# Optimization experiments

Hardware: AMD Instinct MI355X
Metric: run time of the kernel (lower is better)

Reference implementation:

```python
import math
import jax, jax.numpy as jnp
import numpy as np

B, C, N, K = 16, 64, 2048, 20

def setup_inputs() -> dict:
    key = jax.random.key(0)
    x = jax.random.normal(key, (B, C, N), dtype=jnp.float32)
    local_idx = jnp.zeros((B, N), dtype=bool)  # unused in dgcnn variant
    return {"x": x, "k": K, "local_idx": local_idx}

def _gather_points(points, idx):
    # points: (B, N, C), idx: (B, N, k) -> (B, N, k, C)
    return jax.vmap(lambda p, i: p[i])(points, idx)

def reference(x, k, local_idx):
    b, c, n = x.shape
    xt = jnp.swapaxes(x, 1, 2)  # (B, N, C)
    # negative squared pairwise distance: -||xi||^2 + 2 xi.xj - ||xj||^2
    inner = 2.0 * jnp.einsum('bnc,bmc->bnm', xt, xt)
    xx = jnp.sum(xt * xt, axis=-1)  # (B, N)
    pd = -xx[:, :, None] + inner - xx[:, None, :]
    _, idx = jax.lax.top_k(pd, k)  # (B, N, k) nearest neighbors
    knn_x = _gather_points(xt, idx)  # (B, N, k, C)
    # per-channel topk over the k neighbors, then mean
    k2 = math.ceil(k * 2 / 3)
    vals = jax.lax.top_k(jnp.swapaxes(knn_x, 2, 3), k2)[0]  # (B, N, C, k2)
    x1 = jnp.mean(vals, axis=-1)  # (B, N, C)
    # gather smoothed features at neighbor indices
    feat = _gather_points(x1, idx)  # (B, N, k, C)
    x_exp = jnp.broadcast_to(xt[:, :, None, :], (b, n, k, c))
    feature = jnp.concatenate([feat - x_exp, x_exp], axis=-1)  # (B, N, k, 2C)
    feature = jnp.transpose(feature, (0, 3, 1, 2))  # (B, 2C, N, k)
    idx_flat = (idx + jnp.arange(b, dtype=idx.dtype)[:, None, None] * n).reshape(-1)
    return feature, idx_flat
```

## Files before the change

kernel.cpp:

```cpp
#include <hip/hip_runtime.h>
#include <cstdint>
#include <cstddef>
#include <math.h>

#define BB 16
#define CC 64
#define NN 2048
#define KK 20
#define K2 14
#define TQ 8
#define NC 26

__global__ __launch_bounds__(256) void prep_kernel(const float* __restrict__ x,
                                                   float* __restrict__ xt,
                                                   float* __restrict__ xxf,
                                                   double* __restrict__ xxd) {
    __shared__ float s_t[64][65];
    int b = blockIdx.x >> 5;
    int n0 = (blockIdx.x & 31) * 64;
    const float* xb = x + (size_t)b * CC * NN;
    int tid = threadIdx.x;
    int cq = tid >> 6;
    int nl = tid & 63;

#pragma unroll
    for (int r = 0; r < 16; ++r) {
        int c = r * 4 + cq;
        s_t[c][nl] = xb[c * NN + n0 + nl];
    }
    __syncthreads();

#pragma unroll
    for (int r = 0; r < 16; ++r) {
        int n = r * 4 + cq;
        xt[((size_t)b * NN + n0 + n) * CC + nl] = s_t[nl][n];
    }

    if (tid < 64) {
        double s = 0.0;
#pragma unroll
        for (int c = 0; c < CC; ++c) {
            double v = (double)s_t[c][tid];
            s += v * v;
        }
        xxd[b * NN + n0 + tid] = s;
        xxf[b * NN + n0 + tid] = (float)s;
    }
}

__global__ __launch_bounds__(512) void knn_kernel(const float* __restrict__ x,
                                                  const float* __restrict__ xt,
                                                  const float* __restrict__ xxf,
                                                  const double* __restrict__ xxd,
                                                  int* __restrict__ idx_ws,
                                                  float* __restrict__ idx_out) {
    __shared__ float s_pd[TQ][NN];
    __shared__ __align__(16) float s_q[CC][TQ];
    __shared__ float s_sv[TQ][64];
    __shared__ int   s_si[TQ][64];

    int tid = threadIdx.x;
    int b = blockIdx.x >> 8;
    int n0 = (blockIdx.x & 255) * TQ;
    const float* xb = x + (size_t)b * CC * NN;

    { int c = tid >> 3, qq = tid & 7; s_q[c][qq] = xb[c * NN + n0 + qq]; }
    __syncthreads();

    {
        float4 xa = *(const float4*)(xxf + b * NN + n0);
        float4 xc = *(const float4*)(xxf + b * NN + n0 + 4);
        float xxn[TQ] = {xa.x, xa.y, xa.z, xa.w, xc.x, xc.y, xc.z, xc.w};

        int m = tid * 4;
        float acc[TQ][4];
#pragma unroll
        for (int q = 0; q < TQ; ++q)
#pragma unroll
            for (int i = 0; i < 4; ++i) acc[q][i] = 0.f;

        for (int c = 0; c < CC; ++c) {
            float4 xv = *(const float4*)(xb + c * NN + m);
            float4 qa = *(const float4*)(&s_q[c][0]);
            float4 qb = *(const float4*)(&s_q[c][4]);
            float xs[4] = {xv.x, xv.y, xv.z, xv.w};
            float qs[TQ] = {qa.x, qa.y, qa.z, qa.w, qb.x, qb.y, qb.z, qb.w};
#pragma unroll
            for (int q = 0; q < TQ; ++q)
#pragma unroll
                for (int i = 0; i < 4; ++i) acc[q][i] += qs[q] * xs[i];
        }
        float4 xm4 = *(const float4*)(xxf + b * NN + m);
        float xms[4] = {xm4.x, xm4.y, xm4.z, xm4.w};
#pragma unroll
        for (int q = 0; q < TQ; ++q) {
            float4 pdv;
            pdv.x = (2.f * acc[q][0] - xxn[q]) - xms[0];
            pdv.y = (2.f * acc[q][1] - xxn[q]) - xms[1];
            pdv.z = (2.f * acc[q][2] - xxn[q]) - xms[2];
            pdv.w = (2.f * acc[q][3] - xxn[q]) - xms[3];
            *(float4*)(&s_pd[q][m]) = pdv;
        }
    }
    __syncthreads();

    int q = tid >> 6;
    int lane = tid & 63;
    const float* pd = s_pd[q];

    float v[32];
#pragma unroll
    for (int r = 0; r < 32; ++r) v[r] = pd[lane + (r << 6)];

    float lmax = v[0]; int lr = 0;
#pragma unroll
    for (int r = 1; r < 32; ++r)
        if (v[r] > lmax) { lmax = v[r]; lr = r; }

    float sv = lmax;
#pragma unroll
    for (int k = 2; k <= 64; k <<= 1) {
#pragma unroll
        for (int j = k >> 1; j > 0; j >>= 1) {
            float o = __shfl_xor(sv, j);
            bool dird = ((lane & k) == 0);
            bool first = ((lane & j) == 0);
            sv = (first == dird) ? fmaxf(sv, o) : fminf(sv, o);
        }
    }
    float tau = __shfl(sv, 25);

    int cnt = 0;
#pragma unroll
    for (int r = 0; r < 32; ++r) cnt += (v[r] >= tau) ? 1 : 0;
    int incl = cnt;
#pragma unroll
    for (int off = 1; off < 64; off <<= 1) {
        int o = __shfl_up(incl, off);
        if (lane >= off) incl += o;
    }
    int S = __shfl(incl, 63);

    float fv = -INFINITY;
    int fi = 0x7fffffff;
    if (S <= 64) {
        int w = incl - cnt;
#pragma unroll
        for (int r = 0; r < 32; ++r) {
            if (v[r] >= tau) { s_sv[q][w] = v[r]; s_si[q][w] = lane + (r << 6); ++w; }
        }
        if (lane < S) { fv = s_sv[q][lane]; fi = s_si[q][lane]; }
    } else {
        for (int t = 0; t < NC; ++t) {
            float bv = lmax; int bi = lane + (lr << 6);
#pragma unroll
            for (int off = 32; off; off >>= 1) {
                float ov = __shfl_xor(bv, off);
                int oi = __shfl_xor(bi, off);
                if (ov > bv || (ov == bv && oi < bi)) { bv = ov; bi = oi; }
            }
            if (lane == t) { fv = bv; fi = bi; }
            if ((bi & 63) == lane) {
                int rsel = bi >> 6;
#pragma unroll
                for (int r = 0; r < 32; ++r) if (r == rsel) v[r] = -INFINITY;
                lmax = v[0]; lr = 0;
#pragma unroll
                for (int r = 1; r < 32; ++r)
                    if (v[r] > lmax) { lmax = v[r]; lr = r; }
            }
        }
    }

#pragma unroll
    for (int k = 2; k <= 64; k <<= 1) {
#pragma unroll
        for (int j = k >> 1; j > 0; j >>= 1) {
            float ov = __shfl_xor(fv, j);
            int oi = __shfl_xor(fi, j);
            bool dird = ((lane & k) == 0);
            bool first = ((lane & j) == 0);
            bool better = (fv > ov) || (fv == ov && fi < oi);
            if (better != (first == dird)) { fv = ov; fi = oi; }
        }
    }

    float* s_c = (float*)&s_pd[q][0];
    const float* xtb = xt + (size_t)b * NN * CC;
    int nq = n0 + q;

#pragma unroll
    for (int t = 0; t < NC; ++t) {
        int cand = __shfl(fi, t);
        s_c[lane * 27 + t] = xtb[(size_t)cand * CC + lane];
    }

    double accd = 0.0;
    for (int c = 0; c < CC; ++c) {
        double qc = (double)s_q[c][q];
        double cd = (double)s_c[c * 27 + lane];
        accd = fma(qc, cd, accd);
    }

    double val = -INFINITY;
    int idxq = 0x7fffffff;
    if (lane < NC) {
        val = 2.0 * accd - xxd[b * NN + nq] - xxd[b * NN + fi];
        idxq = fi;
    }

#pragma unroll
    for (int k = 2; k <= 32; k <<= 1) {
#pragma unroll
        for (int j = k >> 1; j > 0; j >>= 1) {
            double ov = __shfl_xor(val, j, 32);
            int oi = __shfl_xor(idxq, j, 32);
            bool dird = ((lane & k) == 0);
            bool first = ((lane & j) == 0);
            bool better = (val > ov) || (val == ov && idxq < oi);
            if (better != (first == dird)) { val = ov; idxq = oi; }
        }
    }

    if (lane < KK) {
        size_t obase = ((size_t)b * NN + nq) * KK;
        idx_ws[obase + lane] = idxq;
        idx_out[obase + lane] = (float)(idxq + b * NN);
    }
}

__global__ __launch_bounds__(256) void x1_kernel(const float* __restrict__ xt,
                                                 const int* __restrict__ idx_ws,
                                                 float* __restrict__ x1t) {
    __shared__ int s_idx[16][KK];
    __shared__ float s_out[64][17];
    int tid = threadIdx.x;
    int b = blockIdx.x >> 7;
    int n0 = (blockIdx.x & 127) * 16;
    const float* xtb = xt + (size_t)b * NN * CC;

    for (int i = tid; i < 16 * KK; i += 256)
        s_idx[i / KK][i % KK] = idx_ws[((size_t)b * NN + n0) * KK + i];
    __syncthreads();

    int pl = tid >> 6, c = tid & 63;
#pragma unroll
    for (int it = 0; it < 4; ++it) {
        int nl = it * 4 + pl;
        float vals[KK];
        float sum = 0.f;
#pragma unroll
        for (int j = 0; j < KK; ++j) {
            vals[j] = xtb[(size_t)s_idx[nl][j] * CC + c];
            sum += vals[j];
        }
#pragma unroll
        for (int t = 0; t < KK - K2; ++t) {
            float worst = INFINITY;
            int wj = 0;
#pragma unroll
            for (int j = 0; j < KK; ++j)
                if (vals[j] < worst) { worst = vals[j]; wj = j; }
            sum -= worst;
            vals[wj] = INFINITY;
        }
        s_out[c][nl] = sum / (float)K2;
    }
    __syncthreads();

    int cw = tid >> 2, nw = (tid & 3) * 4;
    float4 v = make_float4(s_out[cw][nw], s_out[cw][nw + 1],
                           s_out[cw][nw + 2], s_out[cw][nw + 3]);
    *(float4*)(&x1t[((size_t)b * CC + cw) * NN + n0 + nw]) = v;
}

__global__ __launch_bounds__(256) void feat_kernel(const float* __restrict__ x,
                                                   const float* __restrict__ x1t,
                                                   const int* __restrict__ idx_ws,
                                                   float* __restrict__ out) {
    int bc = blockIdx.x;
    int b = bc >> 7, ch = bc & 127;
    const float* xb = x + (size_t)b * CC * NN;
    float* o = out + (size_t)bc * NN * KK;
    const int* idxb = idx_ws + (size_t)b * NN * KK;

    if (ch < CC) {
        const float* row = x1t + ((size_t)b * CC + ch) * NN;
        const float* xr = xb + ch * NN;
        for (int it = 0; it < 40; ++it) {
            unsigned e = (it * 256 + threadIdx.x) * 4;
            int4 id4 = *(const int4*)(idxb + e);
            float4 o4;
            o4.x = row[id4.x] - xr[(e    ) / KK];
            o4.y = row[id4.y] - xr[(e + 1) / KK];
            o4.z = row[id4.z] - xr[(e + 2) / KK];
            o4.w = row[id4.w] - xr[(e + 3) / KK];
            *(float4*)(o + e) = o4;
        }
    } else {
        const float* xr = xb + (ch - CC) * NN;
        for (int it = 0; it < 40; ++it) {
            unsigned e = (it * 256 + threadIdx.x) * 4;
            float4 o4;
            o4.x = xr[(e    ) / KK];
            o4.y = xr[(e + 1) / KK];
            o4.z = xr[(e + 2) / KK];
            o4.w = xr[(e + 3) / KK];
            *(float4*)(o + e) = o4;
        }
    }
}

extern "C" void kernel_launch(void* const* d_in, const int* in_sizes, int n_in,
                              void* d_out, int out_size, void* d_ws, size_t ws_size,
                              hipStream_t stream) {
    const float* x = (const float*)d_in[0];
    float* out = (float*)d_out;

    char* ws = (char*)d_ws;
    float* xt   = (float*)ws;
    float* x1t  = (float*)(ws + (size_t)8388608);
    double* xxd = (double*)(ws + (size_t)16777216);
    float* xxf  = (float*)(ws + (size_t)17039360);
    int* idx_ws = (int*)(ws + (size_t)17170432);

    float* idx_out = out + (size_t)BB * 2 * CC * NN * KK;

    prep_kernel<<<BB * (NN / 64), 256, 0, stream>>>(x, xt, xxf, xxd);
    knn_kernel<<<BB * (NN / TQ), 512, 0, stream>>>(x, xt, xxf, xxd, idx_ws, idx_out);
    x1_kernel<<<BB * (NN / 16), 256, 0, stream>>>(xt, idx_ws, x1t);
    feat_kernel<<<BB * 2 * CC, 256, 0, stream>>>(x, x1t, idx_ws, out);
}
```

Before: 660.0 us.

## Compute kNN distance matrix with split-bf16 MFMA and 16 queries per block

The prep kernel now also writes hi/lo bf16 splits of the transposed points. The kNN kernel computes the query-by-all-points inner products with MFMA 16x16x32 bf16 instructions, using three cross products (hi·hi, hi·lo, lo·hi) to approximate fp32. Queries per block rise from 8 to 16 with 1024 threads, and the pd rows are padded. The coarse distances drop the per-query norm, which is constant per row and so does not change the ranking. Candidates are still re-ranked in double precision. Cost: extra prep writes, lower coarse precision, and much more shared memory per block.

Measured after the change: 709.8 us. +7.5%, slower.

```diff
diff --git a/kernel.cpp b/kernel.cpp
--- a/kernel.cpp
+++ b/kernel.cpp
@@ -8,11 +8,24 @@
 #define NN 2048
 #define KK 20
 #define K2 14
-#define TQ 8
+#define TQ 16
 #define NC 26
+#define PDS 2052
+
+typedef unsigned short ushort_t;
+typedef __attribute__((ext_vector_type(8))) short bf16x8;
+typedef __attribute__((ext_vector_type(4))) float f32x4;
+
+__device__ inline ushort_t f2bf_rne(float f) {
+    uint32_t u = __float_as_uint(f);
+    uint32_t r = (u + 0x7FFFu + ((u >> 16) & 1u)) >> 16;
+    return (ushort_t)r;
+}
 
 __global__ __launch_bounds__(256) void prep_kernel(const float* __restrict__ x,
                                                    float* __restrict__ xt,
+                                                   ushort_t* __restrict__ xth,
+                                                   ushort_t* __restrict__ xtl,
                                                    float* __restrict__ xxf,
                                                    double* __restrict__ xxd) {
     __shared__ float s_t[64][65];
@@ -33,7 +46,13 @@
 #pragma unroll
     for (int r = 0; r < 16; ++r) {
         int n = r * 4 + cq;
-        xt[((size_t)b * NN + n0 + n) * CC + nl] = s_t[nl][n];
+        float v = s_t[nl][n];
+        size_t off = ((size_t)b * NN + n0 + n) * CC + nl;
+        xt[off] = v;
+        ushort_t h = f2bf_rne(v);
+        float hv = __uint_as_float((uint32_t)h << 16);
+        xth[off] = h;
+        xtl[off] = f2bf_rne(v - hv);
     }
 
     if (tid < 64) {
@@ -48,65 +67,70 @@
     }
 }
 
-__global__ __launch_bounds__(512) void knn_kernel(const float* __restrict__ x,
-                                                  const float* __restrict__ xt,
-                                                  const float* __restrict__ xxf,
-                                                  const double* __restrict__ xxd,
-                                                  int* __restrict__ idx_ws,
-                                                  float* __restrict__ idx_out) {
-    __shared__ float s_pd[TQ][NN];
-    __shared__ __align__(16) float s_q[CC][TQ];
+__global__ __launch_bounds__(1024) void knn_kernel(const float* __restrict__ xt,
+                                                   const ushort_t* __restrict__ xth,
+                                                   const ushort_t* __restrict__ xtl,
+                                                   const float* __restrict__ xxf,
+                                                   const double* __restrict__ xxd,
+                                                   int* __restrict__ idx_ws,
+                                                   float* __restrict__ idx_out) {
+    __shared__ float s_pd[TQ][PDS];
+    __shared__ float s_qf[TQ][CC];
     __shared__ float s_sv[TQ][64];
     __shared__ int   s_si[TQ][64];
 
     int tid = threadIdx.x;
-    int b = blockIdx.x >> 8;
-    int n0 = (blockIdx.x & 255) * TQ;
-    const float* xb = x + (size_t)b * CC * NN;
-
-    { int c = tid >> 3, qq = tid & 7; s_q[c][qq] = xb[c * NN + n0 + qq]; }
+    int b = blockIdx.x >> 7;
+    int nq0 = (blockIdx.x & 127) * TQ;
+
+    {
+        int q = tid >> 6, c = tid & 63;
+        s_qf[q][c] = xt[((size_t)b * NN + nq0 + q) * CC + c];
+    }
+
+    int w = tid >> 6;
+    int lane = tid & 63;
+    int mrow = lane & 15, quad = lane >> 4;
+
+    {
+        const size_t rowbase = (size_t)b * NN * CC;
+        const ushort_t* Ah = xth + rowbase + (size_t)(nq0 + mrow) * CC + quad * 8;
+        const ushort_t* Al = xtl + rowbase + (size_t)(nq0 + mrow) * CC + quad * 8;
+        bf16x8 ah0 = *(const bf16x8*)(Ah);
+        bf16x8 ah1 = *(const bf16x8*)(Ah + 32);
+        bf16x8 al0 = *(const bf16x8*)(Al);
+        bf16x8 al1 = *(const bf16x8*)(Al + 32);
+
+#pragma unroll
+        for (int t = 0; t < 8; ++t) {
+            int nt = w * 8 + t;
+            int ncol = nt * 16 + mrow;
+            const ushort_t* Bh = xth + rowbase + (size_t)ncol * CC + quad * 8;
+            const ushort_t* Bl = xtl + rowbase + (size_t)ncol * CC + quad * 8;
+            bf16x8 bh0 = *(const bf16x8*)(Bh);
+            bf16x8 bh1 = *(const bf16x8*)(Bh + 32);
+            bf16x8 bl0 = *(const bf16x8*)(Bl);
+            bf16x8 bl1 = *(const bf16x8*)(Bl + 32);
+
+            f32x4 acc = {0.f, 0.f, 0.f, 0.f};
+            acc = __builtin_amdgcn_mfma_f32_16x16x32_bf16(ah0, bh0, acc, 0, 0, 0);
+            acc = __builtin_amdgcn_mfma_f32_16x16x32_bf16(ah1, bh1, acc, 0, 0, 0);
+            acc = __builtin_amdgcn_mfma_f32_16x16x32_bf16(ah0, bl0, acc, 0, 0, 0);
+            acc = __builtin_amdgcn_mfma_f32_16x16x32_bf16(ah1, bl1, acc, 0, 0, 0);
+            acc = __builtin_amdgcn_mfma_f32_16x16x32_bf16(al0, bh0, acc, 0, 0, 0);
+            acc = __builtin_amdgcn_mfma_f32_16x16x32_bf16(al1, bh1, acc, 0, 0, 0);
+
+            float xmv = xxf[b * NN + ncol];
+#pragma unroll
+            for (int r = 0; r < 4; ++r) {
+                int qrow = quad * 4 + r;
+                s_pd[qrow][ncol] = 2.f * acc[r] - xmv;
+            }
+        }
+    }
     __syncthreads();
 
-    {
-        float4 xa = *(const float4*)(xxf + b * NN + n0);
-        float4 xc = *(const float4*)(xxf + b * NN + n0 + 4);
-        float xxn[TQ] = {xa.x, xa.y, xa.z, xa.w, xc.x, xc.y, xc.z, xc.w};
-
-        int m = tid * 4;
-        float acc[TQ][4];
-#pragma unroll
-        for (int q = 0; q < TQ; ++q)
-#pragma unroll
-            for (int i = 0; i < 4; ++i) acc[q][i] = 0.f;
-
-        for (int c = 0; c < CC; ++c) {
-            float4 xv = *(const float4*)(xb + c * NN + m);
-            float4 qa = *(const float4*)(&s_q[c][0]);
-            float4 qb = *(const float4*)(&s_q[c][4]);
-            float xs[4] = {xv.x, xv.y, xv.z, xv.w};
-            float qs[TQ] = {qa.x, qa.y, qa.z, qa.w, qb.x, qb.y, qb.z, qb.w};
-#pragma unroll
-            for (int q = 0; q < TQ; ++q)
-#pragma unroll
-                for (int i = 0; i < 4; ++i) acc[q][i] += qs[q] * xs[i];
-        }
-        float4 xm4 = *(const float4*)(xxf + b * NN + m);
-        float xms[4] = {xm4.x, xm4.y, xm4.z, xm4.w};
-#pragma unroll
-        for (int q = 0; q < TQ; ++q) {
-            float4 pdv;
-            pdv.x = (2.f * acc[q][0] - xxn[q]) - xms[0];
-            pdv.y = (2.f * acc[q][1] - xxn[q]) - xms[1];
-            pdv.z = (2.f * acc[q][2] - xxn[q]) - xms[2];
-            pdv.w = (2.f * acc[q][3] - xxn[q]) - xms[3];
-            *(float4*)(&s_pd[q][m]) = pdv;
-        }
-    }
-    __syncthreads();
-
-    int q = tid >> 6;
-    int lane = tid & 63;
-    const float* pd = s_pd[q];
+    const float* pd = s_pd[w];
 
     float v[32];
 #pragma unroll
@@ -144,12 +168,12 @@
     float fv = -INFINITY;
     int fi = 0x7fffffff;
     if (S <= 64) {
-        int w = incl - cnt;
+        int wr = incl - cnt;
 #pragma unroll
         for (int r = 0; r < 32; ++r) {
-            if (v[r] >= tau) { s_sv[q][w] = v[r]; s_si[q][w] = lane + (r << 6); ++w; }
-        }
-        if (lane < S) { fv = s_sv[q][lane]; fi = s_si[q][lane]; }
+            if (v[r] >= tau) { s_sv[w][wr] = v[r]; s_si[w][wr] = lane + (r << 6); ++wr; }
+        }
+        if (lane < S) { fv = s_sv[w][lane]; fi = s_si[w][lane]; }
     } else {
         for (int t = 0; t < NC; ++t) {
             float bv = lmax; int bi = lane + (lr << 6);
@@ -185,19 +209,18 @@
         }
     }
 
-    float* s_c = (float*)&s_pd[q][0];
-    const float* xtb = xt + (size_t)b * NN * CC;
-    int nq = n0 + q;
+    float* s_c = &s_pd[w][0];
+    int nq = nq0 + w;
 
 #pragma unroll
     for (int t = 0; t < NC; ++t) {
         int cand = __shfl(fi, t);
-        s_c[lane * 27 + t] = xtb[(size_t)cand * CC + lane];
+        s_c[lane * 27 + t] = xt[((size_t)b * NN + cand) * CC + lane];
     }
 
     double accd = 0.0;
     for (int c = 0; c < CC; ++c) {
-        double qc = (double)s_q[c][q];
+        double qc = (double)s_qf[w][c];
         double cd = (double)s_c[c * 27 + lane];
         accd = fma(qc, cd, accd);
     }
@@ -318,16 +341,18 @@
     float* out = (float*)d_out;
 
     char* ws = (char*)d_ws;
-    float* xt   = (float*)ws;
-    float* x1t  = (float*)(ws + (size_t)8388608);
-    double* xxd = (double*)(ws + (size_t)16777216);
-    float* xxf  = (float*)(ws + (size_t)17039360);
-    int* idx_ws = (int*)(ws + (size_t)17170432);
+    float* xt      = (float*)ws;
+    float* x1t     = (float*)(ws + (size_t)8388608);
+    double* xxd    = (double*)(ws + (size_t)16777216);
+    float* xxf     = (float*)(ws + (size_t)17039360);
+    int* idx_ws    = (int*)(ws + (size_t)17170432);
+    ushort_t* xth  = (ushort_t*)(ws + (size_t)20971520);
+    ushort_t* xtl  = (ushort_t*)(ws + (size_t)25165824);
 
     float* idx_out = out + (size_t)BB * 2 * CC * NN * KK;
 
-    prep_kernel<<<BB * (NN / 64), 256, 0, stream>>>(x, xt, xxf, xxd);
-    knn_kernel<<<BB * (NN / TQ), 512, 0, stream>>>(x, xt, xxf, xxd, idx_ws, idx_out);
+    prep_kernel<<<BB * (NN / 64), 256, 0, stream>>>(x, xt, xth, xtl, xxf, xxd);
+    knn_kernel<<<BB * (NN / TQ), 1024, 0, stream>>>(xt, xth, xtl, xxf, xxd, idx_ws, idx_out);
     x1_kernel<<<BB * (NN / 16), 256, 0, stream>>>(xt, idx_ws, x1t);
     feat_kernel<<<BB * 2 * CC, 256, 0, stream>>>(x, x1t, idx_ws, out);
 }
```
